# Kernel optimization log

Measured on AMD Instinct MI355X. Metric: run time of the kernel, lower is better.

The kernel has to match this reference:

```python
import jax, jax.numpy as jnp
import numpy as np

N = 100000
E = 1600000
IN_DIM = 128
HID_DIM = 128
NUM_CLASSES = 40


def setup_inputs() -> dict:
    key = jax.random.key(0)
    k1, k2, k3, k4, k5, k6 = jax.random.split(key, 6)
    x = jax.random.normal(k1, (N, IN_DIM), dtype=jnp.float32)
    e = jax.random.randint(k2, (2, E), 0, N, dtype=jnp.int64)
    s1 = 1.0 / np.sqrt(IN_DIM)
    s2 = 1.0 / np.sqrt(HID_DIM)
    W1 = jax.random.uniform(k3, (IN_DIM, HID_DIM), jnp.float32, -s1, s1)
    b1 = jax.random.uniform(k4, (HID_DIM,), jnp.float32, -s1, s1)
    W2 = jax.random.uniform(k5, (HID_DIM, NUM_CLASSES), jnp.float32, -s2, s2)
    b2 = jax.random.uniform(k6, (NUM_CLASSES,), jnp.float32, -s2, s2)
    return {"x": x, "e": e, "W1": W1, "b1": b1, "W2": W2, "b2": b2}


def _gcn_conv(x, src, dst, norm, W, b, n):
    # linear transform first (PyG GCNConv), then normalized aggregation
    h = x @ W                                    # [N, d_out]
    out = jax.ops.segment_sum(h[src] * norm[:, None], dst, num_segments=n)
    return out + b


def reference(x, e, W1, b1, W2, b2):
    n = x.shape[0]
    loop = jnp.arange(n, dtype=e.dtype)
    src = jnp.concatenate([e[0], loop])          # add self-loops
    dst = jnp.concatenate([e[1], loop])
    deg = jax.ops.segment_sum(jnp.ones_like(dst, dtype=x.dtype), dst, num_segments=n)
    d_inv_sqrt = deg ** -0.5                     # deg >= 1 due to self-loops
    norm = d_inv_sqrt[src] * d_inv_sqrt[dst]     # symmetric normalization
    h = jax.nn.relu(_gcn_conv(x, src, dst, norm, W1, b1, n))
    return _gcn_conv(h, src, dst, norm, W2, b2, n)
```

## Files before the change

kernel.cpp:

```cpp
#include <hip/hip_runtime.h>


typedef unsigned int u32;
typedef unsigned short u16;
typedef __attribute__((ext_vector_type(8))) short short8;
typedef __attribute__((ext_vector_type(4))) float floatx4;

#define CHUNK 4096

static __device__ inline u16 f2bf(float f) {
    u32 u = __float_as_uint(f);
    return (u16)((u + 0x7FFFu + ((u >> 16) & 1u)) >> 16);
}
static __device__ inline u32 pack2(float a, float b) {
    return (u32)f2bf(a) | ((u32)f2bf(b) << 16);
}
static __device__ inline float bflo(u32 u) { return __uint_as_float(u << 16); }
static __device__ inline float bfhi(u32 u) { return __uint_as_float(u & 0xffff0000u); }

static __device__ inline bool detect_is64(const int* e32, int lane) {
    bool nz = e32[2 * lane + 1] != 0;
    return __ballot(nz) == 0ull;
}

__global__ void k_prepW(const float* __restrict__ W1, const float* __restrict__ W2,
                        u16* __restrict__ WTb, u16* __restrict__ W2Tb) {
    int id = blockIdx.x * 256 + threadIdx.x;
    if (id < 16384) {
        int k = id >> 7, c = id & 127;
        WTb[c * 128 + k] = f2bf(W1[id]);
    } else {
        int id2 = id - 16384;
        if (id2 < 6144) {
            int c = id2 >> 7, k = id2 & 127;
            W2Tb[id2] = f2bf(c < 40 ? W2[k * 40 + c] : 0.f);
        }
    }
}

__global__ __launch_bounds__(256) void k_front(const void* __restrict__ e_raw,
                                               int E, int NC, int NB,
                                               int* __restrict__ histG,
                                               const float* __restrict__ X,
                                               const u16* __restrict__ WTb,
                                               u16* __restrict__ H1s, int n) {
    __shared__ u32 smem[64 * 68 + 128 * 68];
    const int tid = threadIdx.x;
    if ((int)blockIdx.x < NC) {
        int* h = (int*)smem;
        h[tid] = 0; h[tid + 256] = 0;
        __syncthreads();
        const int* e32 = (const int*)e_raw;
        bool is64 = detect_is64(e32, tid & 63);
        int c = blockIdx.x;
        int j0 = c * CHUNK, j1 = min(E, j0 + CHUNK);
        for (int j = j0 + tid; j < j1; j += 256) {
            int d = is64 ? (int)((const long long*)e_raw)[E + j] : e32[E + j];
            atomicAdd(&h[d >> 8], 1);
        }
        __syncthreads();
        for (int b = tid; b < NB; b += 256) histG[(size_t)b * NC + c] = h[b];
        return;
    }
    u32* As = smem;
    u32* Bs = smem + 64 * 68;
    const int row0 = ((int)blockIdx.x - NC) * 64;
#pragma unroll
    for (int it = 0; it < 8; it++) {
        int i = tid + it * 256;
        int r = i >> 5;
        int c4 = (i & 31) << 2;
        int gr = row0 + r;
        float4 v = make_float4(0.f, 0.f, 0.f, 0.f);
        if (gr < n) v = *(const float4*)(X + (size_t)gr * 128 + c4);
        uint2 p;
        p.x = pack2(v.x, v.y);
        p.y = pack2(v.z, v.w);
        *(uint2*)&As[r * 68 + (c4 >> 1)] = p;
    }
#pragma unroll
    for (int it = 0; it < 8; it++) {
        int i = tid + it * 256;
        int r = i >> 4;
        int c4 = (i & 15) << 2;
        *(uint4*)&Bs[r * 68 + c4] =
            *(const uint4*)((const u32*)WTb + (size_t)r * 64 + c4);
    }
    __syncthreads();

    const int lane = tid & 63;
    const int wave = tid >> 6;
    const int wr = wave >> 1;
    const int wc = wave & 1;
    const int mrow = lane & 15;
    const int quad = lane >> 4;

    floatx4 acc[2][4] = {};
    for (int k0 = 0; k0 < 128; k0 += 32) {
        int koff = (k0 >> 1) + quad * 4;
        short8 a[2], b[4];
#pragma unroll
        for (int i = 0; i < 2; i++)
            a[i] = *(const short8*)&As[((wr * 2 + i) * 16 + mrow) * 68 + koff];
#pragma unroll
        for (int j = 0; j < 4; j++)
            b[j] = *(const short8*)&Bs[((wc * 4 + j) * 16 + mrow) * 68 + koff];
#pragma unroll
        for (int i = 0; i < 2; i++)
#pragma unroll
            for (int j = 0; j < 4; j++)
                acc[i][j] = __builtin_amdgcn_mfma_f32_16x16x32_bf16(
                    a[i], b[j], acc[i][j], 0, 0, 0);
    }
#pragma unroll
    for (int i = 0; i < 2; i++) {
        int gr0 = row0 + (wr * 2 + i) * 16 + quad * 4;
#pragma unroll
        for (int j = 0; j < 4; j++) {
            int gcol = (wc * 4 + j) * 16 + mrow;
#pragma unroll
            for (int rg = 0; rg < 4; rg++) {
                int grow = gr0 + rg;
                if (grow < n)
                    H1s[(size_t)grow * 128 + gcol] = f2bf(acc[i][j][rg]);
            }
        }
    }
}

__global__ void k_scan1(const int* __restrict__ in, int* __restrict__ out,
                        int* __restrict__ bsum, int n) {
    __shared__ int sh[256];
    int i = blockIdx.x * 256 + threadIdx.x;
    int v = (i < n) ? in[i] : 0;
    sh[threadIdx.x] = v;
    __syncthreads();
    for (int off = 1; off < 256; off <<= 1) {
        int t = (threadIdx.x >= off) ? sh[threadIdx.x - off] : 0;
        __syncthreads();
        sh[threadIdx.x] += t;
        __syncthreads();
    }
    if (i < n) out[i] = sh[threadIdx.x] - v;
    if (threadIdx.x == 255) bsum[blockIdx.x] = sh[255];
}

__global__ void k_scan2(int* __restrict__ bsum, int nb) {
    __shared__ int sh[1024];
    int t = threadIdx.x;
    int v = (t < nb) ? bsum[t] : 0;
    sh[t] = v;
    __syncthreads();
    for (int off = 1; off < 1024; off <<= 1) {
        int u = (t >= off) ? sh[t - off] : 0;
        __syncthreads();
        sh[t] += u;
        __syncthreads();
    }
    if (t < nb) bsum[t] = sh[t] - v;
}

__global__ __launch_bounds__(256) void k_place(const void* __restrict__ e_raw,
                                               const int* __restrict__ histOff,
                                               const int* __restrict__ bsumH,
                                               u32* __restrict__ tmp,
                                               int E, int NB, int NC) {
    __shared__ int cur[512];
    int c = blockIdx.x;
    int t = threadIdx.x;
    for (int b = t; b < NB; b += 256) {
        int idx = b * NC + c;
        cur[b] = histOff[idx] + bsumH[idx >> 8];
    }
    __syncthreads();
    const int* e32 = (const int*)e_raw;
    bool is64 = detect_is64(e32, t & 63);
    int j0 = c * CHUNK, j1 = min(E, j0 + CHUNK);
    for (int j = j0 + t; j < j1; j += 256) {
        int s, d;
        if (is64) {
            s = (int)((const long long*)e_raw)[j];
            d = (int)((const long long*)e_raw)[E + j];
        } else {
            s = e32[j];
            d = e32[E + j];
        }
        int pos = atomicAdd(&cur[d >> 8], 1);
        tmp[pos] = (u32)s | ((u32)(d & 255) << 24);
    }
}

__global__ __launch_bounds__(256) void k_deg(const u32* __restrict__ tmp,
                                             const int* __restrict__ histOff,
                                             const int* __restrict__ bsumH,
                                             int* __restrict__ degI,
                                             float* __restrict__ dinv,
                                             int* __restrict__ rs,
                                             int n, int NB, int NC, int E) {
    __shared__ int cnt[256];
    __shared__ int sh[256];
    int b = blockIdx.x;
    int t = threadIdx.x;
    cnt[t] = 0;
    __syncthreads();
    int i0 = b * NC;
    int seg0 = histOff[i0] + bsumH[i0 >> 8];
    int seg1 = E;
    if (b + 1 < NB) {
        int i1 = (b + 1) * NC;
        seg1 = histOff[i1] + bsumH[i1 >> 8];
    }
    for (int j = seg0 + t; j < seg1; j += 256) atomicAdd(&cnt[tmp[j] >> 24], 1);
    __syncthreads();
    int v = cnt[t];
    sh[t] = v;
    __syncthreads();
    for (int off = 1; off < 256; off <<= 1) {
        int u = (t >= off) ? sh[t - off] : 0;
        __syncthreads();
        sh[t] += u;
        __syncthreads();
    }
    int node = b * 256 + t;
    if (node < n) {
        degI[node] = v;
        dinv[node] = rsqrtf((float)v + 1.0f);
        rs[node] = seg0 + sh[t] - v;
    }
}

__global__ __launch_bounds__(256) void k_bsort(const u32* __restrict__ tmp,
                                               const int* __restrict__ rs,
                                               int* __restrict__ eSrc, int n, int E) {
    __shared__ int rsl[257];
    __shared__ int cur[256];
    int base = blockIdx.x * 256;
    int t = threadIdx.x;
    int node = base + t;
    rsl[t] = (node < n) ? rs[node] : E;
    cur[t] = 0;
    if (t == 0) rsl[256] = (base + 256 < n) ? rs[base + 256] : E;
    __syncthreads();
    int seg0 = rsl[0];
    int seg1 = rsl[256];
    for (int j = seg0 + t; j < seg1; j += 256) {
        u32 rec = tmp[j];
        int dl = rec >> 24;
        int s = (int)(rec & 0x00FFFFFFu);
        int pos = rsl[dl] + atomicAdd(&cur[dl], 1);
        eSrc[pos] = s;
    }
}

__global__ __launch_bounds__(256) void k_gather128(
    const u32* __restrict__ Hb, const int* __restrict__ rs,
    const int* __restrict__ degI, const int* __restrict__ eSrc,
    const float* __restrict__ dinv, const float* __restrict__ b1,
    u32* __restrict__ outb, int n) {
    int wave = threadIdx.x >> 6;
    int lane = threadIdx.x & 63;
    int node = blockIdx.x * 4 + wave;
    if (node >= n) return;
    int start = rs[node];
    int deg = degI[node];
    float ax = 0.f, ay = 0.f;
    for (int base = 0; base < deg; base += 64) {
        int mS = 0;
        float mW = 0.f;
        if (base + lane < deg) { mS = eSrc[start + base + lane]; mW = dinv[mS]; }
        int cnt = min(64, deg - base);
        int t = 0;
        for (; t + 8 <= cnt; t += 8) {
            int s0 = __shfl(mS, t + 0), s1 = __shfl(mS, t + 1);
            int s2 = __shfl(mS, t + 2), s3 = __shfl(mS, t + 3);
            int s4 = __shfl(mS, t + 4), s5 = __shfl(mS, t + 5);
            int s6 = __shfl(mS, t + 6), s7 = __shfl(mS, t + 7);
            float w0 = __shfl(mW, t + 0), w1 = __shfl(mW, t + 1);
            float w2 = __shfl(mW, t + 2), w3 = __shfl(mW, t + 3);
            float w4 = __shfl(mW, t + 4), w5 = __shfl(mW, t + 5);
            float w6 = __shfl(mW, t + 6), w7 = __shfl(mW, t + 7);
            u32 u0 = Hb[(size_t)s0 * 64 + lane];
            u32 u1 = Hb[(size_t)s1 * 64 + lane];
            u32 u2 = Hb[(size_t)s2 * 64 + lane];
            u32 u3 = Hb[(size_t)s3 * 64 + lane];
            u32 u4 = Hb[(size_t)s4 * 64 + lane];
            u32 u5 = Hb[(size_t)s5 * 64 + lane];
            u32 u6 = Hb[(size_t)s6 * 64 + lane];
            u32 u7 = Hb[(size_t)s7 * 64 + lane];
            ax = fmaf(w0, bflo(u0), ax); ay = fmaf(w0, bfhi(u0), ay);
            ax = fmaf(w1, bflo(u1), ax); ay = fmaf(w1, bfhi(u1), ay);
            ax = fmaf(w2, bflo(u2), ax); ay = fmaf(w2, bfhi(u2), ay);
            ax = fmaf(w3, bflo(u3), ax); ay = fmaf(w3, bfhi(u3), ay);
            ax = fmaf(w4, bflo(u4), ax); ay = fmaf(w4, bfhi(u4), ay);
            ax = fmaf(w5, bflo(u5), ax); ay = fmaf(w5, bfhi(u5), ay);
            ax = fmaf(w6, bflo(u6), ax); ay = fmaf(w6, bfhi(u6), ay);
            ax = fmaf(w7, bflo(u7), ax); ay = fmaf(w7, bfhi(u7), ay);
        }
        for (; t < cnt; t++) {
            int s = __shfl(mS, t);
            float w = __shfl(mW, t);
            u32 u = Hb[(size_t)s * 64 + lane];
            ax = fmaf(w, bflo(u), ax); ay = fmaf(w, bfhi(u), ay);
        }
    }
    float di = dinv[node];
    u32 us = Hb[(size_t)node * 64 + lane];
    float inx = fmaf(di, bflo(us), ax);
    float iny = fmaf(di, bfhi(us), ay);
    float2 bv = *(const float2*)(b1 + lane * 2);
    float rx = fmaxf(fmaf(di, inx, bv.x), 0.f);
    float ry = fmaxf(fmaf(di, iny, bv.y), 0.f);
    outb[(size_t)node * 64 + lane] = pack2(rx, ry);
}

__global__ __launch_bounds__(256) void k_gemm2(const u32* __restrict__ A1b,
                                               const u16* __restrict__ W2Tb,
                                               const float* __restrict__ dinv,
                                               u16* __restrict__ H2s, int n) {
    __shared__ u32 As[64 * 68];
    __shared__ u32 Bs[48 * 68];
    const int tid = threadIdx.x;
    const int row0 = blockIdx.x * 64;
#pragma unroll
    for (int it = 0; it < 4; it++) {
        int i = tid + it * 256;
        int r = i >> 4;
        int c4 = (i & 15) << 2;
        int gr = row0 + r;
        uint4 v = make_uint4(0u, 0u, 0u, 0u);
        if (gr < n) v = *(const uint4*)(A1b + (size_t)gr * 64 + c4);
        *(uint4*)&As[r * 68 + c4] = v;
    }
#pragma unroll
    for (int it = 0; it < 3; it++) {
        int i = tid + it * 256;
        int r = i >> 4;
        int c4 = (i & 15) << 2;
        *(uint4*)&Bs[r * 68 + c4] =
            *(const uint4*)((const u32*)W2Tb + (size_t)r * 64 + c4);
    }
    __syncthreads();

    const int lane = tid & 63;
    const int wave = tid >> 6;
    const int mrow = lane & 15;
    const int quad = lane >> 4;

    floatx4 acc[3] = {};
    for (int k0 = 0; k0 < 128; k0 += 32) {
        int koff = (k0 >> 1) + quad * 4;
        short8 a = *(const short8*)&As[(wave * 16 + mrow) * 68 + koff];
#pragma unroll
        for (int j = 0; j < 3; j++) {
            short8 b = *(const short8*)&Bs[(j * 16 + mrow) * 68 + koff];
            acc[j] = __builtin_amdgcn_mfma_f32_16x16x32_bf16(a, b, acc[j], 0, 0, 0);
        }
    }
    int gr0 = row0 + wave * 16 + quad * 4;
    float dv[4];
#pragma unroll
    for (int rg = 0; rg < 4; rg++)
        dv[rg] = (gr0 + rg < n) ? dinv[gr0 + rg] : 0.f;
#pragma unroll
    for (int j = 0; j < 3; j++) {
        int gcol = j * 16 + mrow;
        if (gcol < 40) {
#pragma unroll
            for (int rg = 0; rg < 4; rg++) {
                int grow = gr0 + rg;
                if (grow < n)
                    H2s[(size_t)grow * 40 + gcol] = f2bf(dv[rg] * acc[j][rg]);
            }
        }
    }
}

__global__ __launch_bounds__(256) void k_gather40(
    const u32* __restrict__ H2b, const int* __restrict__ rs,
    const int* __restrict__ degI, const int* __restrict__ eSrc,
    const float* __restrict__ dinv, const float* __restrict__ b2,
    float* __restrict__ out, int n) {
    int wave = threadIdx.x >> 6;
    int lane = threadIdx.x & 63;
    int node = blockIdx.x * 4 + wave;
    if (node >= n) return;
    int start = rs[node];
    int deg = degI[node];
    int g = lane / 20;
    int l = lane - g * 20;
    float ax = 0.f, ay = 0.f;
    for (int base = 0; base < deg; base += 64) {
        int mS = 0;
        if (base + lane < deg) mS = eSrc[start + base + lane];
        int cnt = min(64, deg - base);
        for (int t = 0; t < cnt; t += 3) {
            int e = (t + g) & 63;
            int s = __shfl(mS, e);
            if (g < 3 && t + g < cnt) {
                u32 u = H2b[(size_t)s * 20 + l];
                ax += bflo(u);
                ay += bfhi(u);
            }
        }
    }
    float x1 = __shfl(ax, (lane + 20) & 63), y1 = __shfl(ay, (lane + 20) & 63);
    float x2 = __shfl(ax, (lane + 40) & 63), y2 = __shfl(ay, (lane + 40) & 63);
    if (lane < 20) {
        float di = dinv[node];
        u32 u = H2b[(size_t)node * 20 + l];
        float2 bv = *(const float2*)(b2 + l * 2);
        float ox = fmaf(di, ax + x1 + x2 + bflo(u), bv.x);
        float oy = fmaf(di, ay + y1 + y2 + bfhi(u), bv.y);
        *(float2*)(out + (size_t)node * 40 + l * 2) = make_float2(ox, oy);
    }
}

extern "C" void kernel_launch(void* const* d_in, const int* in_sizes, int n_in,
                              void* d_out, int out_size, void* d_ws, size_t ws_size,
                              hipStream_t stream) {
    const float* x  = (const float*)d_in[0];
    const void*  e  = d_in[1];
    const float* W1 = (const float*)d_in[2];
    const float* b1 = (const float*)d_in[3];
    const float* W2 = (const float*)d_in[4];
    const float* b2 = (const float*)d_in[5];
    float* out = (float*)d_out;

    const int n = in_sizes[0] / 128;
    const int E = in_sizes[1] / 2;
    const int NB = (n + 255) / 256;
    const int NC = (E + CHUNK - 1) / CHUNK;
    const int NH = NB * NC;
    const int nbH = (NH + 255) / 256;
    const int G1 = (n + 63) / 64;

    int*   degI    = (int*)d_ws;
    int*   rs      = degI + n;
    int*   bsumH   = rs + n;
    float* dinv    = (float*)(bsumH + 1024);
    int*   histG   = (int*)(dinv + n);
    int*   histOff = histG + NH;
    size_t off = (size_t)((char*)(histOff + NH) - (char*)d_ws);
    off = (off + 15) & ~(size_t)15;
    u16*   WTb    = (u16*)((char*)d_ws + off);
    u16*   W2Tb   = WTb + 16384;
    off = (size_t)((char*)(W2Tb + 6144) - (char*)d_ws);
    off = (off + 15) & ~(size_t)15;
    u32*   tmp    = (u32*)((char*)d_ws + off);
    int*   eSrc   = (int*)(tmp + (size_t)E);
    u16*   H1s    = (u16*)(eSrc + (size_t)E);
    u32*   H1b    = (u32*)H1s;
    u32*   A1b    = (u32*)(H1s + (size_t)n * 128);
    u16*   H2s    = (u16*)(A1b + (size_t)n * 64);
    u32*   H2b    = (u32*)H2s;

    k_prepW<<<88, 256, 0, stream>>>(W1, W2, WTb, W2Tb);
    k_front<<<NC + G1, 256, 0, stream>>>(e, E, NC, NB, histG, x, WTb, H1s, n);

    k_scan1<<<nbH, 256, 0, stream>>>(histG, histOff, bsumH, NH);
    k_scan2<<<1, 1024, 0, stream>>>(bsumH, nbH);
    k_place<<<NC, 256, 0, stream>>>(e, histOff, bsumH, tmp, E, NB, NC);

    k_deg<<<NB, 256, 0, stream>>>(tmp, histOff, bsumH, degI, dinv, rs,
                                  n, NB, NC, E);
    k_bsort<<<NB, 256, 0, stream>>>(tmp, rs, eSrc, n, E);

    k_gather128<<<(n + 3) / 4, 256, 0, stream>>>(H1b, rs, degI, eSrc, dinv,
                                                 b1, A1b, n);
    k_gemm2<<<(n + 63) / 64, 256, 0, stream>>>(A1b, W2Tb, dinv, H2s, n);
    k_gather40<<<(n + 3) / 4, 256, 0, stream>>>(H2b, rs, degI, eSrc, dinv,
                                                b2, out, n);
}
```

Baseline: 318.7 us.

## Fuse degree count with bucket sort, and layer-1 gather with second GEMM

Merges k_deg and k_bsort into one kernel that reuses the block's scanned row starts as atomic cursors, so the tmp buckets are read in the same block and one launch goes away. Also fuses the 128-wide gather/ReLU into the W2 MFMA GEMM: each wave aggregates 16 nodes straight into shared memory, which removes the A1b intermediate write and read. In exchange the gather now runs with far fewer blocks (n/64 instead of n/4) and each wave processes 16 nodes serially. That lowers parallelism and latency hiding for the memory-bound gather.

```diff
diff --git a/kernel.cpp b/kernel.cpp
--- a/kernel.cpp
+++ b/kernel.cpp
@@ -190,15 +190,17 @@
     }
 }
 
-__global__ __launch_bounds__(256) void k_deg(const u32* __restrict__ tmp,
-                                             const int* __restrict__ histOff,
-                                             const int* __restrict__ bsumH,
-                                             int* __restrict__ degI,
-                                             float* __restrict__ dinv,
-                                             int* __restrict__ rs,
-                                             int n, int NB, int NC, int E) {
+__global__ __launch_bounds__(256) void k_degsort(const u32* __restrict__ tmp,
+                                                 const int* __restrict__ histOff,
+                                                 const int* __restrict__ bsumH,
+                                                 int* __restrict__ degI,
+                                                 float* __restrict__ dinv,
+                                                 int* __restrict__ rs,
+                                                 int* __restrict__ eSrc,
+                                                 int n, int NB, int NC, int E) {
     __shared__ int cnt[256];
     __shared__ int sh[256];
+    __shared__ int cur[256];
     int b = blockIdx.x;
     int t = threadIdx.x;
     cnt[t] = 0;
@@ -221,116 +223,35 @@
         sh[t] += u;
         __syncthreads();
     }
+    int myStart = seg0 + sh[t] - v;
+    cur[t] = myStart;
     int node = b * 256 + t;
     if (node < n) {
         degI[node] = v;
         dinv[node] = rsqrtf((float)v + 1.0f);
-        rs[node] = seg0 + sh[t] - v;
-    }
-}
-
-__global__ __launch_bounds__(256) void k_bsort(const u32* __restrict__ tmp,
-                                               const int* __restrict__ rs,
-                                               int* __restrict__ eSrc, int n, int E) {
-    __shared__ int rsl[257];
-    __shared__ int cur[256];
-    int base = blockIdx.x * 256;
-    int t = threadIdx.x;
-    int node = base + t;
-    rsl[t] = (node < n) ? rs[node] : E;
-    cur[t] = 0;
-    if (t == 0) rsl[256] = (base + 256 < n) ? rs[base + 256] : E;
-    __syncthreads();
-    int seg0 = rsl[0];
-    int seg1 = rsl[256];
+        rs[node] = myStart;
+    }
+    __syncthreads();
     for (int j = seg0 + t; j < seg1; j += 256) {
         u32 rec = tmp[j];
         int dl = rec >> 24;
         int s = (int)(rec & 0x00FFFFFFu);
-        int pos = rsl[dl] + atomicAdd(&cur[dl], 1);
+        int pos = atomicAdd(&cur[dl], 1);
         eSrc[pos] = s;
     }
 }
 
-__global__ __launch_bounds__(256) void k_gather128(
+__global__ __launch_bounds__(256) void k_gg2(
     const u32* __restrict__ Hb, const int* __restrict__ rs,
     const int* __restrict__ degI, const int* __restrict__ eSrc,
     const float* __restrict__ dinv, const float* __restrict__ b1,
-    u32* __restrict__ outb, int n) {
-    int wave = threadIdx.x >> 6;
-    int lane = threadIdx.x & 63;
-    int node = blockIdx.x * 4 + wave;
-    if (node >= n) return;
-    int start = rs[node];
-    int deg = degI[node];
-    float ax = 0.f, ay = 0.f;
-    for (int base = 0; base < deg; base += 64) {
-        int mS = 0;
-        float mW = 0.f;
-        if (base + lane < deg) { mS = eSrc[start + base + lane]; mW = dinv[mS]; }
-        int cnt = min(64, deg - base);
-        int t = 0;
-        for (; t + 8 <= cnt; t += 8) {
-            int s0 = __shfl(mS, t + 0), s1 = __shfl(mS, t + 1);
-            int s2 = __shfl(mS, t + 2), s3 = __shfl(mS, t + 3);
-            int s4 = __shfl(mS, t + 4), s5 = __shfl(mS, t + 5);
-            int s6 = __shfl(mS, t + 6), s7 = __shfl(mS, t + 7);
-            float w0 = __shfl(mW, t + 0), w1 = __shfl(mW, t + 1);
-            float w2 = __shfl(mW, t + 2), w3 = __shfl(mW, t + 3);
-            float w4 = __shfl(mW, t + 4), w5 = __shfl(mW, t + 5);
-            float w6 = __shfl(mW, t + 6), w7 = __shfl(mW, t + 7);
-            u32 u0 = Hb[(size_t)s0 * 64 + lane];
-            u32 u1 = Hb[(size_t)s1 * 64 + lane];
-            u32 u2 = Hb[(size_t)s2 * 64 + lane];
-            u32 u3 = Hb[(size_t)s3 * 64 + lane];
-            u32 u4 = Hb[(size_t)s4 * 64 + lane];
-            u32 u5 = Hb[(size_t)s5 * 64 + lane];
-            u32 u6 = Hb[(size_t)s6 * 64 + lane];
-            u32 u7 = Hb[(size_t)s7 * 64 + lane];
-            ax = fmaf(w0, bflo(u0), ax); ay = fmaf(w0, bfhi(u0), ay);
-            ax = fmaf(w1, bflo(u1), ax); ay = fmaf(w1, bfhi(u1), ay);
-            ax = fmaf(w2, bflo(u2), ax); ay = fmaf(w2, bfhi(u2), ay);
-            ax = fmaf(w3, bflo(u3), ax); ay = fmaf(w3, bfhi(u3), ay);
-            ax = fmaf(w4, bflo(u4), ax); ay = fmaf(w4, bfhi(u4), ay);
-            ax = fmaf(w5, bflo(u5), ax); ay = fmaf(w5, bfhi(u5), ay);
-            ax = fmaf(w6, bflo(u6), ax); ay = fmaf(w6, bfhi(u6), ay);
-            ax = fmaf(w7, bflo(u7), ax); ay = fmaf(w7, bfhi(u7), ay);
-        }
-        for (; t < cnt; t++) {
-            int s = __shfl(mS, t);
-            float w = __shfl(mW, t);
-            u32 u = Hb[(size_t)s * 64 + lane];
-            ax = fmaf(w, bflo(u), ax); ay = fmaf(w, bfhi(u), ay);
-        }
-    }
-    float di = dinv[node];
-    u32 us = Hb[(size_t)node * 64 + lane];
-    float inx = fmaf(di, bflo(us), ax);
-    float iny = fmaf(di, bfhi(us), ay);
-    float2 bv = *(const float2*)(b1 + lane * 2);
-    float rx = fmaxf(fmaf(di, inx, bv.x), 0.f);
-    float ry = fmaxf(fmaf(di, iny, bv.y), 0.f);
-    outb[(size_t)node * 64 + lane] = pack2(rx, ry);
-}
-
-__global__ __launch_bounds__(256) void k_gemm2(const u32* __restrict__ A1b,
-                                               const u16* __restrict__ W2Tb,
-                                               const float* __restrict__ dinv,
-                                               u16* __restrict__ H2s, int n) {
+    const u16* __restrict__ W2Tb, u16* __restrict__ H2s, int n) {
     __shared__ u32 As[64 * 68];
     __shared__ u32 Bs[48 * 68];
     const int tid = threadIdx.x;
+    const int lane = tid & 63;
+    const int wave = tid >> 6;
     const int row0 = blockIdx.x * 64;
-#pragma unroll
-    for (int it = 0; it < 4; it++) {
-        int i = tid + it * 256;
-        int r = i >> 4;
-        int c4 = (i & 15) << 2;
-        int gr = row0 + r;
-        uint4 v = make_uint4(0u, 0u, 0u, 0u);
-        if (gr < n) v = *(const uint4*)(A1b + (size_t)gr * 64 + c4);
-        *(uint4*)&As[r * 68 + c4] = v;
-    }
 #pragma unroll
     for (int it = 0; it < 3; it++) {
         int i = tid + it * 256;
@@ -339,13 +260,63 @@
         *(uint4*)&Bs[r * 68 + c4] =
             *(const uint4*)((const u32*)W2Tb + (size_t)r * 64 + c4);
     }
-    __syncthreads();
-
-    const int lane = tid & 63;
-    const int wave = tid >> 6;
+    float2 bv = *(const float2*)(b1 + lane * 2);
+    for (int i = 0; i < 16; i++) {
+        int node = row0 + wave * 16 + i;
+        if (node >= n) break;
+        int start = rs[node];
+        int deg = degI[node];
+        float ax = 0.f, ay = 0.f;
+        for (int base = 0; base < deg; base += 64) {
+            int mS = 0;
+            float mW = 0.f;
+            if (base + lane < deg) { mS = eSrc[start + base + lane]; mW = dinv[mS]; }
+            int cnt = min(64, deg - base);
+            int t = 0;
+            for (; t + 8 <= cnt; t += 8) {
+                int s0 = __shfl(mS, t + 0), s1 = __shfl(mS, t + 1);
+                int s2 = __shfl(mS, t + 2), s3 = __shfl(mS, t + 3);
+                int s4 = __shfl(mS, t + 4), s5 = __shfl(mS, t + 5);
+                int s6 = __shfl(mS, t + 6), s7 = __shfl(mS, t + 7);
+                float w0 = __shfl(mW, t + 0), w1 = __shfl(mW, t + 1);
+                float w2 = __shfl(mW, t + 2), w3 = __shfl(mW, t + 3);
+                float w4 = __shfl(mW, t + 4), w5 = __shfl(mW, t + 5);
+                float w6 = __shfl(mW, t + 6), w7 = __shfl(mW, t + 7);
+                u32 u0 = Hb[(size_t)s0 * 64 + lane];
+                u32 u1 = Hb[(size_t)s1 * 64 + lane];
+                u32 u2 = Hb[(size_t)s2 * 64 + lane];
+                u32 u3 = Hb[(size_t)s3 * 64 + lane];
+                u32 u4 = Hb[(size_t)s4 * 64 + lane];
+                u32 u5 = Hb[(size_t)s5 * 64 + lane];
+                u32 u6 = Hb[(size_t)s6 * 64 + lane];
+                u32 u7 = Hb[(size_t)s7 * 64 + lane];
+                ax = fmaf(w0, bflo(u0), ax); ay = fmaf(w0, bfhi(u0), ay);
+                ax = fmaf(w1, bflo(u1), ax); ay = fmaf(w1, bfhi(u1), ay);
+                ax = fmaf(w2, bflo(u2), ax); ay = fmaf(w2, bfhi(u2), ay);
+                ax = fmaf(w3, bflo(u3), ax); ay = fmaf(w3, bfhi(u3), ay);
+                ax = fmaf(w4, bflo(u4), ax); ay = fmaf(w4, bfhi(u4), ay);
+                ax = fmaf(w5, bflo(u5), ax); ay = fmaf(w5, bfhi(u5), ay);
+                ax = fmaf(w6, bflo(u6), ax); ay = fmaf(w6, bfhi(u6), ay);
+                ax = fmaf(w7, bflo(u7), ax); ay = fmaf(w7, bfhi(u7), ay);
+            }
+            for (; t < cnt; t++) {
+                int s = __shfl(mS, t);
+                float w = __shfl(mW, t);
+                u32 u = Hb[(size_t)s * 64 + lane];
+                ax = fmaf(w, bflo(u), ax); ay = fmaf(w, bfhi(u), ay);
+            }
+        }
+        float di = dinv[node];
+        u32 us = Hb[(size_t)node * 64 + lane];
+        float inx = fmaf(di, bflo(us), ax);
+        float iny = fmaf(di, bfhi(us), ay);
+        float rx = fmaxf(fmaf(di, inx, bv.x), 0.f);
+        float ry = fmaxf(fmaf(di, iny, bv.y), 0.f);
+        As[(wave * 16 + i) * 68 + lane] = pack2(rx, ry);
+    }
+    __syncthreads();
     const int mrow = lane & 15;
     const int quad = lane >> 4;
-
     floatx4 acc[3] = {};
     for (int k0 = 0; k0 < 128; k0 += 32) {
         int koff = (k0 >> 1) + quad * 4;
@@ -450,8 +421,7 @@
     int*   eSrc   = (int*)(tmp + (size_t)E);
     u16*   H1s    = (u16*)(eSrc + (size_t)E);
     u32*   H1b    = (u32*)H1s;
-    u32*   A1b    = (u32*)(H1s + (size_t)n * 128);
-    u16*   H2s    = (u16*)(A1b + (size_t)n * 64);
+    u16*   H2s    = (u16*)(H1s + (size_t)n * 128);
     u32*   H2b    = (u32*)H2s;
 
     k_prepW<<<88, 256, 0, stream>>>(W1, W2, WTb, W2Tb);
@@ -461,13 +431,11 @@
     k_scan2<<<1, 1024, 0, stream>>>(bsumH, nbH);
     k_place<<<NC, 256, 0, stream>>>(e, histOff, bsumH, tmp, E, NB, NC);
 
-    k_deg<<<NB, 256, 0, stream>>>(tmp, histOff, bsumH, degI, dinv, rs,
-                                  n, NB, NC, E);
-    k_bsort<<<NB, 256, 0, stream>>>(tmp, rs, eSrc, n, E);
-
-    k_gather128<<<(n + 3) / 4, 256, 0, stream>>>(H1b, rs, degI, eSrc, dinv,
-                                                 b1, A1b, n);
-    k_gemm2<<<(n + 63) / 64, 256, 0, stream>>>(A1b, W2Tb, dinv, H2s, n);
+    k_degsort<<<NB, 256, 0, stream>>>(tmp, histOff, bsumH, degI, dinv, rs,
+                                      eSrc, n, NB, NC, E);
+
+    k_gg2<<<(n + 63) / 64, 256, 0, stream>>>(H1b, rs, degI, eSrc, dinv,
+                                             b1, W2Tb, H2s, n);
     k_gather40<<<(n + 3) / 4, 256, 0, stream>>>(H2b, rs, degI, eSrc, dinv,
                                                 b2, out, n);
 }
```

New measurement: 338.3 us. 1.06x slower.
